# Performance work log

Measured on AMD Instinct MI355X. Metric: run time of the kernel, lower is better.

The kernel has to match this reference:

```python
import jax, jax.numpy as jnp
import numpy as np


def setup_inputs() -> dict:
    key = jax.random.key(0)
    kq, kk, kv = jax.random.split(key, 3)
    B, S, H, D = 2, 2048, 16, 64
    q = jax.random.normal(kq, (B, S, H, D), dtype=jnp.float32)
    k = jax.random.normal(kk, (B, S, H, D), dtype=jnp.float32)
    v = jax.random.normal(kv, (B, S, H, D), dtype=jnp.float32)
    # additive key padding mask, [B,1,1,K]; 0 = unmasked, -inf = masked
    key_padding_mask = jnp.zeros((B, 1, 1, S), dtype=jnp.float32)
    return {"q": q, "k": k, "v": v, "key_padding_mask": key_padding_mask}


def reference(q, k, v, key_padding_mask):
    # q,k,v: [B, S, H, D]; key_padding_mask: [B,1,1,K] additive
    head_dim = q.shape[-1]
    softmax_scale = 1.0 / np.sqrt(head_dim).astype(np.float32)
    # [B, H, Q, K] logits with additive mask
    logits = jnp.einsum('bqhd,bkhd->bhqk', q, k) * softmax_scale + key_padding_mask
    attn = jax.nn.softmax(logits, axis=-1)
    # dropout p=0.0 -> identity in eval mode
    out = jnp.einsum('bhqk,bkhd->bqhd', attn, v)
    return out
```

## Files before the change

kernel.cpp:

```cpp
#include <hip/hip_runtime.h>
#include <hip/hip_bf16.h>


typedef __attribute__((ext_vector_type(8))) short bf16x8;
typedef __attribute__((ext_vector_type(4))) short bf16x4;
typedef __attribute__((ext_vector_type(4))) float f32x4;

#define B_ 2
#define S_ 2048
#define H_ 16
#define D_ 64
#define BQ 128
#define BK 64
#define NT (S_ / BK)
#define LDK 72
#define ROWSZ (H_ * D_)

#define LOG2E  1.44269504088896340736f
#define SCALE2 (0.125f * LOG2E)

__device__ __forceinline__ unsigned pack2(float a, float b) {
    union { __hip_bfloat162 h; unsigned u; } x;
    x.h = __float22bfloat162_rn(make_float2(a, b));
    return x.u;
}

__device__ __forceinline__ float fexp2(float x) {
#if __has_builtin(__builtin_amdgcn_exp2f)
    return __builtin_amdgcn_exp2f(x);
#else
    return __expf(x * 0.69314718055994531f);
#endif
}

__device__ __forceinline__ f32x4 mfma16(bf16x4 a, bf16x4 b, f32x4 c) {
#if __has_builtin(__builtin_amdgcn_mfma_f32_16x16x16bf16_1k)
    return __builtin_amdgcn_mfma_f32_16x16x16bf16_1k(a, b, c, 0, 0, 0);
#else
    bf16x8 a8 = {a[0], a[1], a[2], a[3], 0, 0, 0, 0};
    bf16x8 b8 = {b[0], b[1], b[2], b[3], 0, 0, 0, 0};
    return __builtin_amdgcn_mfma_f32_16x16x32_bf16(a8, b8, c, 0, 0, 0);
#endif
}

__global__ __launch_bounds__(512, 4)
void fattn_kernel(const float* __restrict__ qg,
                  const float* __restrict__ kg,
                  const float* __restrict__ vg,
                  const float* __restrict__ maskg,
                  float* __restrict__ outg)
{
    __shared__ __attribute__((aligned(16))) ushort Ks[2][BK * LDK];
    __shared__ __attribute__((aligned(16))) ushort Vt[2][D_ * LDK];
    __shared__ __attribute__((aligned(16))) float  Em[S_];

    const int qt = blockIdx.x, h = blockIdx.y, b = blockIdx.z;
    const int tid = threadIdx.x;
    const int w = tid >> 6, lane = tid & 63, g = lane >> 4, l15 = lane & 15;

    {
        float4 mv = *(const float4*)(maskg + (size_t)b * S_ + tid * 4);
        *(float4*)&Em[tid * 4] = make_float4(mv.x * LOG2E, mv.y * LOG2E,
                                             mv.z * LOG2E, mv.w * LOG2E);
    }

    const int qrow = qt * BQ + w * 16 + l15;
    const float* qp = qg + (size_t)(b * S_ + qrow) * ROWSZ + h * D_;
    bf16x8 qf[2];
#pragma unroll
    for (int half = 0; half < 2; ++half) {
        float4 f0 = *(const float4*)(qp + half * 32 + g * 8);
        float4 f1 = *(const float4*)(qp + half * 32 + g * 8 + 4);
        union { bf16x8 v; uint4 u; } x;
        x.u = make_uint4(pack2(f0.x * SCALE2, f0.y * SCALE2),
                         pack2(f0.z * SCALE2, f0.w * SCALE2),
                         pack2(f1.x * SCALE2, f1.y * SCALE2),
                         pack2(f1.z * SCALE2, f1.w * SCALE2));
        qf[half] = x.v;
    }

    const int skey16 = tid >> 4;
    const int sd4    = (tid & 15) * 4;
    const int svd    = lane;
    const int svk8   = w * 8;
    const int vc0 = (w >> 1) * 4 + 16 * ((2 * w) & 3);
    const int vc1 = (w >> 1) * 4 + 16 * ((2 * w + 1) & 3);

    const size_t kvbase = (size_t)b * S_ * ROWSZ + h * D_;

    float4 kpre0, kpre1;
    float  vpre[8];
    auto prefetch = [&](int kt) {
        const float* kb = kg + kvbase + (size_t)kt * BK * ROWSZ;
        kpre0 = *(const float4*)(kb + (size_t)skey16 * ROWSZ + sd4);
        kpre1 = *(const float4*)(kb + (size_t)(skey16 + 32) * ROWSZ + sd4);
        const float* vb = vg + kvbase + (size_t)kt * BK * ROWSZ + svd;
#pragma unroll
        for (int i = 0; i < 8; ++i) vpre[i] = vb[(size_t)(svk8 + i) * ROWSZ];
    };
    auto stage = [&](int buf) {
        *(uint2*)&Ks[buf][skey16 * LDK + sd4] =
            make_uint2(pack2(kpre0.x, kpre0.y), pack2(kpre0.z, kpre0.w));
        *(uint2*)&Ks[buf][(skey16 + 32) * LDK + sd4] =
            make_uint2(pack2(kpre1.x, kpre1.y), pack2(kpre1.z, kpre1.w));
        *(uint2*)&Vt[buf][svd * LDK + vc0] =
            make_uint2(pack2(vpre[0], vpre[1]), pack2(vpre[2], vpre[3]));
        *(uint2*)&Vt[buf][svd * LDK + vc1] =
            make_uint2(pack2(vpre[4], vpre[5]), pack2(vpre[6], vpre[7]));
    };

    float m_r = -1e30f, l_r = 0.0f;
    f32x4 o_acc[4];
#pragma unroll
    for (int t = 0; t < 4; ++t) o_acc[t] = (f32x4){0.f, 0.f, 0.f, 0.f};

    prefetch(0);
    stage(0);
    __syncthreads();

    for (int kt = 0; kt < NT; ++kt) {
        const int cur = kt & 1;
        if (kt + 1 < NT) prefetch(kt + 1);

        const ushort* ks = Ks[cur];
        float sv[4][4];
#pragma unroll
        for (int t = 0; t < 4; ++t) {
            f32x4 acc = *(const f32x4*)&Em[kt * BK + t * 16 + g * 4];
            bf16x8 kf0 = *(const bf16x8*)&ks[(t * 16 + l15) * LDK + g * 8];
            bf16x8 kf1 = *(const bf16x8*)&ks[(t * 16 + l15) * LDK + 32 + g * 8];
            acc = __builtin_amdgcn_mfma_f32_16x16x32_bf16(kf0, qf[0], acc, 0, 0, 0);
            acc = __builtin_amdgcn_mfma_f32_16x16x32_bf16(kf1, qf[1], acc, 0, 0, 0);
            sv[t][0] = acc[0]; sv[t][1] = acc[1]; sv[t][2] = acc[2]; sv[t][3] = acc[3];
        }

        float cm = sv[0][0];
#pragma unroll
        for (int t = 0; t < 4; ++t)
#pragma unroll
            for (int r = 0; r < 4; ++r) cm = fmaxf(cm, sv[t][r]);
        cm = fmaxf(cm, __shfl_xor(cm, 16));
        cm = fmaxf(cm, __shfl_xor(cm, 32));
        const float newm = fmaxf(m_r, cm);
        const float alpha = fexp2(m_r - newm);
        float rs = 0.f;
#pragma unroll
        for (int t = 0; t < 4; ++t)
#pragma unroll
            for (int r = 0; r < 4; ++r) {
                float p = fexp2(sv[t][r] - newm);
                sv[t][r] = p;
                rs += p;
            }
        l_r = l_r * alpha + rs;
        m_r = newm;
#pragma unroll
        for (int t = 0; t < 4; ++t) {
            o_acc[t][0] *= alpha; o_acc[t][1] *= alpha;
            o_acc[t][2] *= alpha; o_acc[t][3] *= alpha;
        }

        bf16x4 pf[4];
#pragma unroll
        for (int c = 0; c < 4; ++c) {
            union { bf16x4 v; uint2 u; } x;
            x.u = make_uint2(pack2(sv[c][0], sv[c][1]), pack2(sv[c][2], sv[c][3]));
            pf[c] = x.v;
        }

        const ushort* vt = Vt[cur];
#pragma unroll
        for (int t2 = 0; t2 < 4; ++t2) {
#pragma unroll
            for (int c2 = 0; c2 < 2; ++c2) {
                bf16x8 vv = *(const bf16x8*)&vt[(t2 * 16 + l15) * LDK + g * 16 + c2 * 8];
                bf16x4 vlo = {vv[0], vv[1], vv[2], vv[3]};
                bf16x4 vhi = {vv[4], vv[5], vv[6], vv[7]};
                o_acc[t2] = mfma16(vlo, pf[2 * c2],     o_acc[t2]);
                o_acc[t2] = mfma16(vhi, pf[2 * c2 + 1], o_acc[t2]);
            }
        }

        if (kt + 1 < NT) stage(cur ^ 1);
        __syncthreads();
    }

    l_r += __shfl_xor(l_r, 16);
    l_r += __shfl_xor(l_r, 32);
    const float inv = 1.0f / l_r;
    float* op = outg + (size_t)(b * S_ + qrow) * ROWSZ + h * D_;
#pragma unroll
    for (int t2 = 0; t2 < 4; ++t2)
#pragma unroll
        for (int r = 0; r < 4; ++r)
            op[t2 * 16 + g * 4 + r] = o_acc[t2][r] * inv;
}

extern "C" void kernel_launch(void* const* d_in, const int* in_sizes, int n_in,
                              void* d_out, int out_size, void* d_ws, size_t ws_size,
                              hipStream_t stream) {
    dim3 grid(S_ / BQ, H_, B_);
    fattn_kernel<<<grid, dim3(512), 0, stream>>>(
        (const float*)d_in[0], (const float*)d_in[1], (const float*)d_in[2],
        (const float*)d_in[3], (float*)d_out);
}
```

Measured before the change: 155.1 us.

## Process two query sub-tiles per wave and swizzle V transpose layout

Doubles the query block to 256 rows so each wave handles two 16-row query sub-tiles and reuses every K and V fragment read from shared memory for both. It also replaces the split V-transpose store with a single 16-byte store into an XOR-swizzled layout, with matching swizzled reads in the PV loop, to reduce LDS bank conflicts. The cost is higher register pressure (launch bounds drop to 2 blocks per SM) and half as many blocks, 256 in total, which may underfill the GPU.

```diff
diff --git a/kernel.cpp b/kernel.cpp
--- a/kernel.cpp
+++ b/kernel.cpp
@@ -10,7 +10,7 @@
 #define S_ 2048
 #define H_ 16
 #define D_ 64
-#define BQ 128
+#define BQ 256
 #define BK 64
 #define NT (S_ / BK)
 #define LDK 72
@@ -43,7 +43,7 @@
 #endif
 }
 
-__global__ __launch_bounds__(512, 4)
+__global__ __launch_bounds__(512, 2)
 void fattn_kernel(const float* __restrict__ qg,
                   const float* __restrict__ kg,
                   const float* __restrict__ vg,
@@ -57,6 +57,7 @@
     const int qt = blockIdx.x, h = blockIdx.y, b = blockIdx.z;
     const int tid = threadIdx.x;
     const int w = tid >> 6, lane = tid & 63, g = lane >> 4, l15 = lane & 15;
+    const int gh = g >> 1, glo = g & 1, h3 = l15 >> 3;
 
     {
         float4 mv = *(const float4*)(maskg + (size_t)b * S_ + tid * 4);
@@ -64,27 +65,29 @@
                                              mv.z * LOG2E, mv.w * LOG2E);
     }
 
-    const int qrow = qt * BQ + w * 16 + l15;
-    const float* qp = qg + (size_t)(b * S_ + qrow) * ROWSZ + h * D_;
-    bf16x8 qf[2];
-#pragma unroll
-    for (int half = 0; half < 2; ++half) {
-        float4 f0 = *(const float4*)(qp + half * 32 + g * 8);
-        float4 f1 = *(const float4*)(qp + half * 32 + g * 8 + 4);
-        union { bf16x8 v; uint4 u; } x;
-        x.u = make_uint4(pack2(f0.x * SCALE2, f0.y * SCALE2),
-                         pack2(f0.z * SCALE2, f0.w * SCALE2),
-                         pack2(f1.x * SCALE2, f1.y * SCALE2),
-                         pack2(f1.z * SCALE2, f1.w * SCALE2));
-        qf[half] = x.v;
+    bf16x8 qf[2][2];
+#pragma unroll
+    for (int s = 0; s < 2; ++s) {
+        const int qrow = qt * BQ + w * 32 + s * 16 + l15;
+        const float* qp = qg + (size_t)(b * S_ + qrow) * ROWSZ + h * D_;
+#pragma unroll
+        for (int half = 0; half < 2; ++half) {
+            float4 f0 = *(const float4*)(qp + half * 32 + g * 8);
+            float4 f1 = *(const float4*)(qp + half * 32 + g * 8 + 4);
+            union { bf16x8 v; uint4 u; } x;
+            x.u = make_uint4(pack2(f0.x * SCALE2, f0.y * SCALE2),
+                             pack2(f0.z * SCALE2, f0.w * SCALE2),
+                             pack2(f1.x * SCALE2, f1.y * SCALE2),
+                             pack2(f1.z * SCALE2, f1.w * SCALE2));
+            qf[s][half] = x.v;
+        }
     }
 
     const int skey16 = tid >> 4;
     const int sd4    = (tid & 15) * 4;
     const int svd    = lane;
     const int svk8   = w * 8;
-    const int vc0 = (w >> 1) * 4 + 16 * ((2 * w) & 3);
-    const int vc1 = (w >> 1) * 4 + 16 * ((2 * w + 1) & 3);
+    const int vphys  = (w ^ ((lane >> 3) & 7)) * 8;
 
     const size_t kvbase = (size_t)b * S_ * ROWSZ + h * D_;
 
@@ -103,81 +106,93 @@
             make_uint2(pack2(kpre0.x, kpre0.y), pack2(kpre0.z, kpre0.w));
         *(uint2*)&Ks[buf][(skey16 + 32) * LDK + sd4] =
             make_uint2(pack2(kpre1.x, kpre1.y), pack2(kpre1.z, kpre1.w));
-        *(uint2*)&Vt[buf][svd * LDK + vc0] =
-            make_uint2(pack2(vpre[0], vpre[1]), pack2(vpre[2], vpre[3]));
-        *(uint2*)&Vt[buf][svd * LDK + vc1] =
-            make_uint2(pack2(vpre[4], vpre[5]), pack2(vpre[6], vpre[7]));
+        *(uint4*)&Vt[buf][svd * LDK + vphys] =
+            make_uint4(pack2(vpre[0], vpre[1]), pack2(vpre[2], vpre[3]),
+                       pack2(vpre[4], vpre[5]), pack2(vpre[6], vpre[7]));
     };
 
-    float m_r = -1e30f, l_r = 0.0f;
-    f32x4 o_acc[4];
-#pragma unroll
-    for (int t = 0; t < 4; ++t) o_acc[t] = (f32x4){0.f, 0.f, 0.f, 0.f};
+    float m_r[2] = {-1e30f, -1e30f}, l_r[2] = {0.0f, 0.0f};
+    f32x4 o_acc[2][4];
+#pragma unroll
+    for (int s = 0; s < 2; ++s)
+#pragma unroll
+        for (int t = 0; t < 4; ++t) o_acc[s][t] = (f32x4){0.f, 0.f, 0.f, 0.f};
 
     prefetch(0);
     stage(0);
     __syncthreads();
 
+    const int koff = l15 * LDK + g * 8;
+    const int vbase = l15 * LDK + glo * 4;
+
     for (int kt = 0; kt < NT; ++kt) {
         const int cur = kt & 1;
         if (kt + 1 < NT) prefetch(kt + 1);
 
         const ushort* ks = Ks[cur];
-        float sv[4][4];
+        float sv[2][4][4];
 #pragma unroll
         for (int t = 0; t < 4; ++t) {
-            f32x4 acc = *(const f32x4*)&Em[kt * BK + t * 16 + g * 4];
-            bf16x8 kf0 = *(const bf16x8*)&ks[(t * 16 + l15) * LDK + g * 8];
-            bf16x8 kf1 = *(const bf16x8*)&ks[(t * 16 + l15) * LDK + 32 + g * 8];
-            acc = __builtin_amdgcn_mfma_f32_16x16x32_bf16(kf0, qf[0], acc, 0, 0, 0);
-            acc = __builtin_amdgcn_mfma_f32_16x16x32_bf16(kf1, qf[1], acc, 0, 0, 0);
-            sv[t][0] = acc[0]; sv[t][1] = acc[1]; sv[t][2] = acc[2]; sv[t][3] = acc[3];
-        }
-
-        float cm = sv[0][0];
-#pragma unroll
-        for (int t = 0; t < 4; ++t)
-#pragma unroll
-            for (int r = 0; r < 4; ++r) cm = fmaxf(cm, sv[t][r]);
-        cm = fmaxf(cm, __shfl_xor(cm, 16));
-        cm = fmaxf(cm, __shfl_xor(cm, 32));
-        const float newm = fmaxf(m_r, cm);
-        const float alpha = fexp2(m_r - newm);
-        float rs = 0.f;
-#pragma unroll
-        for (int t = 0; t < 4; ++t)
-#pragma unroll
-            for (int r = 0; r < 4; ++r) {
-                float p = fexp2(sv[t][r] - newm);
-                sv[t][r] = p;
-                rs += p;
-            }
-        l_r = l_r * alpha + rs;
-        m_r = newm;
-#pragma unroll
-        for (int t = 0; t < 4; ++t) {
-            o_acc[t][0] *= alpha; o_acc[t][1] *= alpha;
-            o_acc[t][2] *= alpha; o_acc[t][3] *= alpha;
-        }
-
-        bf16x4 pf[4];
-#pragma unroll
-        for (int c = 0; c < 4; ++c) {
-            union { bf16x4 v; uint2 u; } x;
-            x.u = make_uint2(pack2(sv[c][0], sv[c][1]), pack2(sv[c][2], sv[c][3]));
-            pf[c] = x.v;
+            const f32x4 em = *(const f32x4*)&Em[kt * BK + t * 16 + g * 4];
+            bf16x8 kf0 = *(const bf16x8*)&ks[t * 16 * LDK + koff];
+            bf16x8 kf1 = *(const bf16x8*)&ks[t * 16 * LDK + koff + 32];
+#pragma unroll
+            for (int s = 0; s < 2; ++s) {
+                f32x4 acc = em;
+                acc = __builtin_amdgcn_mfma_f32_16x16x32_bf16(kf0, qf[s][0], acc, 0, 0, 0);
+                acc = __builtin_amdgcn_mfma_f32_16x16x32_bf16(kf1, qf[s][1], acc, 0, 0, 0);
+                sv[s][t][0] = acc[0]; sv[s][t][1] = acc[1];
+                sv[s][t][2] = acc[2]; sv[s][t][3] = acc[3];
+            }
+        }
+
+        bf16x4 pf[2][4];
+#pragma unroll
+        for (int s = 0; s < 2; ++s) {
+            float cm = sv[s][0][0];
+#pragma unroll
+            for (int t = 0; t < 4; ++t)
+#pragma unroll
+                for (int r = 0; r < 4; ++r) cm = fmaxf(cm, sv[s][t][r]);
+            cm = fmaxf(cm, __shfl_xor(cm, 16));
+            cm = fmaxf(cm, __shfl_xor(cm, 32));
+            const float newm = fmaxf(m_r[s], cm);
+            const float alpha = fexp2(m_r[s] - newm);
+            float rs = 0.f;
+#pragma unroll
+            for (int t = 0; t < 4; ++t)
+#pragma unroll
+                for (int r = 0; r < 4; ++r) {
+                    float p = fexp2(sv[s][t][r] - newm);
+                    sv[s][t][r] = p;
+                    rs += p;
+                }
+            l_r[s] = l_r[s] * alpha + rs;
+            m_r[s] = newm;
+#pragma unroll
+            for (int t = 0; t < 4; ++t) {
+                o_acc[s][t][0] *= alpha; o_acc[s][t][1] *= alpha;
+                o_acc[s][t][2] *= alpha; o_acc[s][t][3] *= alpha;
+            }
+#pragma unroll
+            for (int c = 0; c < 4; ++c) {
+                union { bf16x4 v; uint2 u; } x;
+                x.u = make_uint2(pack2(sv[s][c][0], sv[s][c][1]),
+                                 pack2(sv[s][c][2], sv[s][c][3]));
+                pf[s][c] = x.v;
+            }
         }
 
         const ushort* vt = Vt[cur];
 #pragma unroll
         for (int t2 = 0; t2 < 4; ++t2) {
-#pragma unroll
-            for (int c2 = 0; c2 < 2; ++c2) {
-                bf16x8 vv = *(const bf16x8*)&vt[(t2 * 16 + l15) * LDK + g * 16 + c2 * 8];
-                bf16x4 vlo = {vv[0], vv[1], vv[2], vv[3]};
-                bf16x4 vhi = {vv[4], vv[5], vv[6], vv[7]};
-                o_acc[t2] = mfma16(vlo, pf[2 * c2],     o_acc[t2]);
-                o_acc[t2] = mfma16(vhi, pf[2 * c2 + 1], o_acc[t2]);
+            const int e = (2 * t2 + h3) & 7;
+#pragma unroll
+            for (int c = 0; c < 4; ++c) {
+                const int physu = (2 * c + gh) ^ e;
+                bf16x4 vf = *(const bf16x4*)&vt[t2 * 16 * LDK + vbase + physu * 8];
+                o_acc[0][t2] = mfma16(vf, pf[0][c], o_acc[0][t2]);
+                o_acc[1][t2] = mfma16(vf, pf[1][c], o_acc[1][t2]);
             }
         }
 
@@ -185,15 +200,20 @@
         __syncthreads();
     }
 
-    l_r += __shfl_xor(l_r, 16);
-    l_r += __shfl_xor(l_r, 32);
-    const float inv = 1.0f / l_r;
-    float* op = outg + (size_t)(b * S_ + qrow) * ROWSZ + h * D_;
-#pragma unroll
-    for (int t2 = 0; t2 < 4; ++t2)
-#pragma unroll
-        for (int r = 0; r < 4; ++r)
-            op[t2 * 16 + g * 4 + r] = o_acc[t2][r] * inv;
+#pragma unroll
+    for (int s = 0; s < 2; ++s) {
+        float lv = l_r[s];
+        lv += __shfl_xor(lv, 16);
+        lv += __shfl_xor(lv, 32);
+        const float inv = 1.0f / lv;
+        const int qrow = qt * BQ + w * 32 + s * 16 + l15;
+        float* op = outg + (size_t)(b * S_ + qrow) * ROWSZ + h * D_;
+#pragma unroll
+        for (int t2 = 0; t2 < 4; ++t2)
+#pragma unroll
+            for (int r = 0; r < 4; ++r)
+                op[t2 * 16 + g * 4 + r] = o_acc[s][t2][r] * inv;
+    }
 }
 
 extern "C" void kernel_launch(void* const* d_in, const int* in_sizes, int n_in,
```

Result: no change. 158.2 us (+2.0%).
